# Kernel optimization log

Hardware: AMD Instinct MI355X
Metric: run time of the kernel (lower is better)

Reference implementation:

```python
import jax, jax.numpy as jnp
import numpy as np
from functools import partial

NUM_ITERS = 3
NUM_CAPS = 8      # primary capsule count
NUM_CLASSES = 10
OUT_CH = 16       # digit capsule dim
INPUT_SIZE = 32 * 6 * 6  # 1152 primary capsule units per capsule map


def squash(s, axis=-1):
    # faithful to non_linear_squashing: s * (||s||^2/(1+||s||^2)) / (||s||+1e-10)
    norm_sqr = jnp.sum(s * s, axis=axis, keepdims=True)
    scale = jnp.sqrt(norm_sqr) + 1e-10
    mag = norm_sqr / (1.0 + norm_sqr)
    return s * mag / scale


def conv2d(x, w, b, stride):
    y = jax.lax.conv_general_dilated(
        x, w, window_strides=(stride, stride), padding='VALID',
        dimension_numbers=('NCHW', 'OIHW', 'NCHW'))
    return y + b[None, :, None, None]


def setup_inputs() -> dict:
    key = jax.random.key(0)
    ks = jax.random.split(key, 6)
    B = 256
    x = jax.random.normal(ks[0], (B, 1, 28, 28), dtype=jnp.float32)
    conv_w = jax.random.normal(ks[1], (256, 1, 9, 9), dtype=jnp.float32) * 0.05
    conv_b = jax.random.normal(ks[2], (256,), dtype=jnp.float32) * 0.05
    # 8 primary capsule conv units (256->32 each) fused into one 256->256 conv
    prim_w = jax.random.normal(ks[3], (NUM_CAPS * 32, 256, 9, 9), dtype=jnp.float32) * 0.02
    prim_b = jax.random.normal(ks[4], (NUM_CAPS * 32,), dtype=jnp.float32) * 0.02
    # digit routing weights (input_size, num_classes, out_channels, num_capsules)
    digit_w = jax.random.normal(ks[5], (INPUT_SIZE, NUM_CLASSES, OUT_CH, NUM_CAPS), dtype=jnp.float32)
    return {'x': x, 'conv_w': conv_w, 'conv_b': conv_b,
            'prim_w': prim_w, 'prim_b': prim_b, 'digit_w': digit_w}


def reference(x, conv_w, conv_b, prim_w, prim_b, digit_w):
    B = x.shape[0]
    # conv stack: 1->256 k9 s1 + ReLU  (28 -> 20); pool is MaxPool2d(1,1) = identity
    h = jax.nn.relu(conv2d(x, conv_w, conv_b, stride=1))  # (B,256,20,20)
    # primary capsules: 8 convs 256->32 k9 s2, no activation (nl_activation=False)
    p = conv2d(h, prim_w, prim_b, stride=2)               # (B,256,6,6)
    u = p.reshape(B, NUM_CAPS, -1)                        # (B,8,1152)
    u = squash(u, axis=-1)
    # digit layer with dynamic routing
    # u_i: (B, IS, 8);  u_j_i[b,i,c,o] = sum_k W[i,c,o,k] * u_i[b,i,k]
    u_i = jnp.transpose(u, (0, 2, 1))                     # (B,1152,8)
    u_j_i = jnp.einsum('icok,bik->bico', digit_w, u_i)    # (B,1152,10,16)
    b_ij = jnp.zeros((INPUT_SIZE, NUM_CLASSES), dtype=x.dtype)
    out = None
    for _ in range(NUM_ITERS):
        c_ij = jax.nn.softmax(b_ij, axis=0)               # softmax over input capsules (dim=1 in torch)
        s_j = jnp.einsum('ic,bico->bco', c_ij, u_j_i)     # (B,10,16)
        # original squashes (B,1,C,16,1) along dim=2 == the CLASS axis
        out = squash(s_j, axis=1)                         # (B,10,16)
        # agreement: mean over batch of <u_j_i, v_j>
        u_v = jnp.einsum('bico,bco->ic', u_j_i, out) / B  # (1152,10)
        b_ij = b_ij + u_v
    # torch returns out.squeeze(1) with shape (B, C, 16, 1)
    return out[..., None]
```

## Files before the change

kernel.cpp:

```cpp
#include <hip/hip_runtime.h>
#include <cstdint>
#include <cstddef>


typedef __attribute__((ext_vector_type(8))) short short8;
typedef __attribute__((ext_vector_type(4))) float f32x4;

#define PHALF 2359296

__device__ __forceinline__ unsigned short f2bf_rn(float x) {
    unsigned u = __float_as_uint(x);
    unsigned r = (u + 0x7fffu + ((u >> 16) & 1u)) >> 16;
    return (unsigned short)r;
}

__global__ void k_pre(const float* __restrict__ x, const float* __restrict__ cw,
                      const float* __restrict__ cb, const float* __restrict__ w2,
                      unsigned short* __restrict__ h, unsigned short* __restrict__ wt) {
    __shared__ float sh[3376];
    int blk = blockIdx.x, t = threadIdx.x;
    if (blk < 2048) {
        float* img = sh;
        float* wsm = sh + 784;
        int b = blk >> 3, ocg = blk & 7;
        for (int idx = t; idx < 784; idx += 256) img[idx] = x[b * 784 + idx];
        for (int idx = t; idx < 2592; idx += 256) wsm[idx] = cw[ocg * 2592 + idx];
        __syncthreads();
        int oc_l = t & 31, g = t >> 5;
        int oc = ocg * 32 + oc_l;
        float bias = cb[oc];
        const float* wp = &wsm[oc_l * 81];
        for (int q = g; q < 100; q += 8) {
            int py = q / 5, qx = (q % 5) * 4;
            float a0 = bias, a1 = bias, a2 = bias, a3 = bias;
            #pragma unroll
            for (int ky = 0; ky < 9; ky++) {
                const float* ir = &img[(py + ky) * 28 + qx];
                float r[12];
                #pragma unroll
                for (int j = 0; j < 12; j++) r[j] = ir[j];
                #pragma unroll
                for (int kx = 0; kx < 9; kx++) {
                    float w = wp[ky * 9 + kx];
                    a0 += r[kx] * w; a1 += r[kx + 1] * w;
                    a2 += r[kx + 2] * w; a3 += r[kx + 3] * w;
                }
            }
            float v[4] = { fmaxf(a0, 0.f), fmaxf(a1, 0.f), fmaxf(a2, 0.f), fmaxf(a3, 0.f) };
            size_t base = ((size_t)b * 400 + py * 20 + qx) * 256 + oc;
            #pragma unroll
            for (int j = 0; j < 4; j++)
                h[base + (size_t)j * 256] = f2bf_rn(v[j]);
        }
    } else {
        int m2 = blk - 2048;
        int oc = m2 >> 3, icg = m2 & 7;
        float* lw2 = sh;
        for (int idx = t; idx < 2592; idx += 256) {
            int ic_l = idx / 81, k = idx % 81;
            lw2[idx] = w2[((size_t)oc * 256 + icg * 32 + ic_l) * 81 + k];
        }
        __syncthreads();
        for (int idx = t; idx < 324; idx += 256) {
            int k = idx >> 2, sl = idx & 3;
            unsigned short hi8[8];
            #pragma unroll
            for (int j = 0; j < 8; j++)
                hi8[j] = f2bf_rn(lw2[(sl * 8 + j) * 81 + k]);
            size_t o = ((size_t)(k * 256 + oc)) * 256 + icg * 32 + sl * 8;
            *(uint4*)&wt[o] = *(uint4*)hi8;
        }
    }
}

__global__ __launch_bounds__(256, 4) void k_conv2m(
    const unsigned short* __restrict__ h,
    const unsigned short* __restrict__ wt,
    float* __restrict__ p0, float* __restrict__ p1,
    float* __restrict__ p2, float* __restrict__ p3)
{
    __shared__ unsigned short smem[14336];
    const int t = threadIdx.x;
    const int w = t >> 6, l = t & 63;
    const int mb = blockIdx.x, nb = blockIdx.y, zz = blockIdx.z;
    const int half = zz >> 1, seg = zz & 1;

    const unsigned short* src;
    int nld, sbase;
    unsigned rowbase[8];
    if (w < 2) {
        src = h; nld = 6; sbase = w * 3072;
        #pragma unroll
        for (int ld = 0; ld < 6; ld++) {
            int row = w * 48 + ld * 8 + (l >> 3);
            int c = l & 7;
            int g = c ^ (row & 7);
            int P = mb * 96 + row;
            int b = P / 36, o = P % 36;
            int oy = o / 6, ox = o % 6;
            rowbase[ld] = (unsigned)((b * 400 + oy * 40 + ox * 2) * 256 + half * 128 + g * 8);
        }
    } else {
        src = wt; nld = 8; sbase = 6144 + (w - 2) * 4096;
        #pragma unroll
        for (int ld = 0; ld < 8; ld++) {
            int oc = (w - 2) * 64 + ld * 8 + (l >> 3);
            int c = l & 7;
            int g = c ^ (oc & 7);
            rowbase[ld] = (unsigned)((nb * 128 + oc) * 256 + half * 128 + g * 8);
        }
    }

    const int wm = w & 1, wn = w >> 1;
    const int lane16 = l & 15, q = l >> 4;

    f32x4 acc[3][4] = {};

    const int pos0 = seg ? 41 : 0;
    const int pos1 = seg ? 81 : 41;
    for (int pos = pos0; pos < pos1; ++pos) {
        const int ky = pos / 9, kx = pos - ky * 9;
        const unsigned kbase = (w < 2) ? (unsigned)((ky * 20 + kx) * 256)
                                       : (unsigned)(pos * 65536);
        for (int icc = 0; icc < 2; ++icc) {
            const unsigned kofs = kbase + icc * 64;
            __syncthreads();
            for (int ld = 0; ld < nld; ld++) {
                __builtin_amdgcn_global_load_lds(
                    (const __attribute__((address_space(1))) unsigned int*)(const void*)(src + rowbase[ld] + kofs),
                    (__attribute__((address_space(3))) unsigned int*)(void*)(smem + sbase + ld * 512),
                    16, 0, 0);
            }
            __syncthreads();
            #pragma unroll
            for (int ic2 = 0; ic2 < 2; ic2++) {
                short8 a[3], b[4];
                #pragma unroll
                for (int mt = 0; mt < 3; mt++) {
                    int pixL = wm * 48 + mt * 16 + lane16;
                    int ps = (ic2 * 4 + q) ^ (pixL & 7);
                    a[mt] = *(const short8*)(smem + pixL * 64 + ps * 8);
                }
                #pragma unroll
                for (int nt = 0; nt < 4; nt++) {
                    int ocL = wn * 64 + nt * 16 + lane16;
                    int ps = (ic2 * 4 + q) ^ (ocL & 7);
                    b[nt] = *(const short8*)(smem + 6144 + ocL * 64 + ps * 8);
                }
                #pragma unroll
                for (int mt = 0; mt < 3; mt++)
                    #pragma unroll
                    for (int nt = 0; nt < 4; nt++)
                        acc[mt][nt] = __builtin_amdgcn_mfma_f32_16x16x32_bf16(a[mt], b[nt], acc[mt][nt], 0, 0, 0);
            }
        }
    }

    #pragma unroll
    for (int mt = 0; mt < 3; mt++) {
        int pixG = mb * 96 + wm * 48 + mt * 16 + q * 4;
        int b = pixG / 36, p36 = pixG % 36;
        #pragma unroll
        for (int nt = 0; nt < 4; nt++) {
            int oc = nb * 128 + wn * 64 + nt * 16 + lane16;
            float* pout = (zz == 0) ? p0 : (zz == 1) ? p1 : (zz == 2) ? p2 : p3;
            *(f32x4*)&pout[((size_t)(b * 256 + oc)) * 36 + p36] = acc[mt][nt];
        }
    }
}

__global__ void k_sq1dw(const float* __restrict__ q0, const float* __restrict__ q1,
                        const float* __restrict__ q2, const float* __restrict__ q3,
                        const float* __restrict__ prim_b, float* __restrict__ U,
                        const float* __restrict__ dw, float* __restrict__ dwT2) {
    __shared__ float red[4];
    int blk = blockIdx.x, t = threadIdx.x;
    if (blk < 2048) {
        int b = blk >> 3, cap = blk & 7;
        size_t base = ((size_t)b * 256 + cap * 32) * 36;
        const float* pa = q0 + base;
        const float* pb = q1 + base;
        const float* pc = q2 + base;
        const float* pd = q3 + base;
        float v[5];
        float ss = 0.f;
        #pragma unroll
        for (int j = 0; j < 5; j++) {
            int idx = t + j * 256;
            if (idx < 1152) {
                int ch_l = idx / 36;
                float val = pa[idx] + pb[idx] + pc[idx] + pd[idx] + prim_b[cap * 32 + ch_l];
                v[j] = val; ss += val * val;
            } else v[j] = 0.f;
        }
        for (int off = 32; off; off >>= 1) ss += __shfl_down(ss, off);
        if ((t & 63) == 0) red[t >> 6] = ss;
        __syncthreads();
        float n2 = red[0] + red[1] + red[2] + red[3];
        float f = (n2 / (1.0f + n2)) / (sqrtf(n2) + 1e-10f);
        #pragma unroll
        for (int j = 0; j < 5; j++) {
            int idx = t + j * 256;
            if (idx < 1152) U[(size_t)b * 9216 + idx * 8 + cap] = v[j] * f;
        }
    } else {
        int co = blk - 2048;
        int c = co >> 4, o = co & 15;
        const float* base = dw + c * 128 + o * 8;
        float* out = dwT2 + (size_t)co * 9216;
        for (int idx = t; idx < 9216; idx += 256) {
            int i = idx >> 3, k = idx & 7;
            out[idx] = base[(size_t)i * 1280 + k];
        }
    }
}

__global__ void k_softmax(const float* __restrict__ bij, float* __restrict__ csm) {
    __shared__ float red[4];
    int c = blockIdx.x, t = threadIdx.x;
    float vals[5];
    float mx = -1e30f;
    #pragma unroll
    for (int j = 0; j < 5; j++) {
        int i = t + j * 256;
        vals[j] = (i < 1152) ? bij[i * 10 + c] : -1e30f;
        mx = fmaxf(mx, vals[j]);
    }
    for (int off = 32; off; off >>= 1) mx = fmaxf(mx, __shfl_down(mx, off));
    if ((t & 63) == 0) red[t >> 6] = mx;
    __syncthreads();
    mx = fmaxf(fmaxf(red[0], red[1]), fmaxf(red[2], red[3]));
    __syncthreads();
    float s = 0.f;
    #pragma unroll
    for (int j = 0; j < 5; j++) {
        int i = t + j * 256;
        vals[j] = (i < 1152) ? expf(vals[j] - mx) : 0.f;
        s += vals[j];
    }
    for (int off = 32; off; off >>= 1) s += __shfl_down(s, off);
    if ((t & 63) == 0) red[t >> 6] = s;
    __syncthreads();
    s = red[0] + red[1] + red[2] + red[3];
    float inv = 1.0f / s;
    #pragma unroll
    for (int j = 0; j < 5; j++) {
        int i = t + j * 256;
        if (i < 1152) csm[i * 10 + c] = vals[j] * inv;
    }
}

__global__ __launch_bounds__(256) void k_gemm1(const float* __restrict__ U,
                                               const float* __restrict__ dwT2,
                                               const float* __restrict__ csm,
                                               float* __restrict__ part,
                                               int uniform) {
    __shared__ float Us[32 * 36];
    __shared__ float WsT[5120];
    __shared__ float cl[360];
    int mb = blockIdx.x, kc = blockIdx.y, t = threadIdx.x;
    int tc = t & 15, tb = t >> 4;
    if (!uniform)
        for (int idx = t; idx < 360; idx += 256) cl[idx] = csm[kc * 360 + idx];
    const float uscale = 1.0f / 1152.0f;
    float acc[2][10] = {};
    for (int ks = 0; ks < 9; ks++) {
        __syncthreads();
        {
            int bb = t >> 3, k4 = t & 7;
            *(float4*)&Us[bb * 36 + k4 * 4] =
                *(const float4*)&U[(size_t)(mb * 32 + bb) * 9216 + kc * 288 + ks * 32 + k4 * 4];
        }
        #pragma unroll
        for (int pass = 0; pass < 5; pass++) {
            int s = t + pass * 256;
            int co = s >> 3, p = s & 7;
            int kq = p ^ (co & 7);
            int ikl = ks * 32 + kq * 4;
            float4 v = *(const float4*)&dwT2[(size_t)co * 9216 + kc * 288 + ikl];
            float sc = uniform ? uscale : cl[(ikl >> 3) * 10 + (co >> 4)];
            v.x *= sc; v.y *= sc; v.z *= sc; v.w *= sc;
            *(float4*)&WsT[s * 4] = v;
        }
        __syncthreads();
        float a0[32], a1[32];
        #pragma unroll
        for (int kq = 0; kq < 8; kq++) {
            float4 v0 = *(const float4*)&Us[(tb * 2) * 36 + kq * 4];
            float4 v1 = *(const float4*)&Us[(tb * 2 + 1) * 36 + kq * 4];
            a0[kq * 4 + 0] = v0.x; a0[kq * 4 + 1] = v0.y; a0[kq * 4 + 2] = v0.z; a0[kq * 4 + 3] = v0.w;
            a1[kq * 4 + 0] = v1.x; a1[kq * 4 + 1] = v1.y; a1[kq * 4 + 2] = v1.z; a1[kq * 4 + 3] = v1.w;
        }
        #pragma unroll
        for (int j = 0; j < 10; j++) {
            int co = tc + 16 * j;
            int cx = co & 7, cbase = co * 32;
            #pragma unroll
            for (int kq = 0; kq < 8; kq++) {
                float4 wv = *(const float4*)&WsT[cbase + ((kq ^ cx) << 2)];
                acc[0][j] += a0[kq * 4 + 0] * wv.x; acc[0][j] += a0[kq * 4 + 1] * wv.y;
                acc[0][j] += a0[kq * 4 + 2] * wv.z; acc[0][j] += a0[kq * 4 + 3] * wv.w;
                acc[1][j] += a1[kq * 4 + 0] * wv.x; acc[1][j] += a1[kq * 4 + 1] * wv.y;
                acc[1][j] += a1[kq * 4 + 2] * wv.z; acc[1][j] += a1[kq * 4 + 3] * wv.w;
            }
        }
    }
    #pragma unroll
    for (int r = 0; r < 2; r++)
        #pragma unroll
        for (int j = 0; j < 10; j++)
            part[(size_t)kc * 40960 + (mb * 32 + tb * 2 + r) * 160 + tc + 16 * j] = acc[r][j];
}

__global__ void k_redsq(const float* __restrict__ part, float* __restrict__ out,
                        float* __restrict__ outT, int writeT) {
    __shared__ float sl[160];
    __shared__ float n2s[16];
    int b = blockIdx.x, t = threadIdx.x;
    float s = 0.f;
    if (t < 160) {
        for (int kc = 0; kc < 32; kc++) s += part[(size_t)kc * 40960 + b * 160 + t];
        sl[t] = s;
    }
    __syncthreads();
    if (t < 16) {
        float n2 = 0.f;
        #pragma unroll
        for (int c = 0; c < 10; c++) { float v = sl[c * 16 + t]; n2 += v * v; }
        n2s[t] = n2;
    }
    __syncthreads();
    if (t < 160) {
        float n2 = n2s[t & 15];
        float f = (n2 / (1.0f + n2)) / (sqrtf(n2) + 1e-10f);
        float r = s * f;
        out[(size_t)b * 160 + t] = r;
        if (writeT) outT[(size_t)t * 256 + b] = r;
    }
}

__global__ __launch_bounds__(256) void k_g2uv(const float* __restrict__ U,
                                              const float* __restrict__ outTg,
                                              const float* __restrict__ dw,
                                              float* __restrict__ bij,
                                              int first) {
    __shared__ float UsT[1024];
    __shared__ float OsT[5120];
    __shared__ float dwl[5120];
    __shared__ float sb[320];
    int blk = blockIdx.x, t = threadIdx.x;
    int tc = t & 15, tm = t >> 4;
    for (int idx = t; idx < 5120; idx += 256)
        dwl[idx] = dw[(size_t)blk * 5120 + idx];
    float acc[2][10] = {};
    for (int bs = 0; bs < 256; bs += 32) {
        __syncthreads();
        {
            int r = t >> 3, c4 = t & 7;
            float4 v = *(const float4*)&U[(size_t)(bs + r) * 9216 + blk * 32 + c4 * 4];
            int hi = (r >> 2), lo = (r & 3);
            int m0 = c4 * 4;
            UsT[(m0 + 0) * 32 + ((hi ^ ((m0 + 0) & 7)) << 2) + lo] = v.x;
            UsT[(m0 + 1) * 32 + ((hi ^ ((m0 + 1) & 7)) << 2) + lo] = v.y;
            UsT[(m0 + 2) * 32 + ((hi ^ ((m0 + 2) & 7)) << 2) + lo] = v.z;
            UsT[(m0 + 3) * 32 + ((hi ^ ((m0 + 3) & 7)) << 2) + lo] = v.w;
        }
        #pragma unroll
        for (int pass = 0; pass < 5; pass++) {
            int s = t + pass * 256;
            int co = s >> 3, p = s & 7;
            int kq = p ^ (co & 7);
            *(float4*)&OsT[s * 4] =
                *(const float4*)&outTg[(size_t)co * 256 + bs + kq * 4];
        }
        __syncthreads();
        float a0[32], a1[32];
        int m0 = tm * 2, m1 = tm * 2 + 1;
        #pragma unroll
        for (int kq = 0; kq < 8; kq++) {
            float4 v0 = *(const float4*)&UsT[m0 * 32 + ((kq ^ (m0 & 7)) << 2)];
            float4 v1 = *(const float4*)&UsT[m1 * 32 + ((kq ^ (m1 & 7)) << 2)];
            a0[kq * 4 + 0] = v0.x; a0[kq * 4 + 1] = v0.y; a0[kq * 4 + 2] = v0.z; a0[kq * 4 + 3] = v0.w;
            a1[kq * 4 + 0] = v1.x; a1[kq * 4 + 1] = v1.y; a1[kq * 4 + 2] = v1.z; a1[kq * 4 + 3] = v1.w;
        }
        #pragma unroll
        for (int j = 0; j < 10; j++) {
            int co = tc + 16 * j;
            int cx = co & 7, cbase = co * 32;
            #pragma unroll
            for (int kq = 0; kq < 8; kq++) {
                float4 wv = *(const float4*)&OsT[cbase + ((kq ^ cx) << 2)];
                acc[0][j] += a0[kq * 4 + 0] * wv.x; acc[0][j] += a0[kq * 4 + 1] * wv.y;
                acc[0][j] += a0[kq * 4 + 2] * wv.z; acc[0][j] += a0[kq * 4 + 3] * wv.w;
                acc[1][j] += a1[kq * 4 + 0] * wv.x; acc[1][j] += a1[kq * 4 + 1] * wv.y;
                acc[1][j] += a1[kq * 4 + 2] * wv.z; acc[1][j] += a1[kq * 4 + 3] * wv.w;
            }
        }
    }
    #pragma unroll
    for (int r = 0; r < 2; r++) {
        int ik_l = tm * 2 + r;
        int i_l = ik_l >> 3, k = ik_l & 7;
        #pragma unroll
        for (int j = 0; j < 10; j++) {
            float v = acc[r][j] * dwl[i_l * 1280 + (j * 16 + tc) * 8 + k];
            v += __shfl_down(v, 8, 16);
            v += __shfl_down(v, 4, 16);
            v += __shfl_down(v, 2, 16);
            v += __shfl_down(v, 1, 16);
            if (tc == 0) sb[ik_l * 10 + j] = v;
        }
    }
    __syncthreads();
    if (t < 40) {
        int i_l = t / 10, c = t % 10;
        float s = 0.f;
        #pragma unroll
        for (int kk = 0; kk < 8; kk++) s += sb[(i_l * 8 + kk) * 10 + c];
        size_t o = (size_t)(blk * 4 + i_l) * 10 + c;
        float v = s * (1.0f / 256.0f);
        bij[o] = first ? v : (bij[o] + v);
    }
}

extern "C" void kernel_launch(void* const* d_in, const int* in_sizes, int n_in,
                              void* d_out, int out_size, void* d_ws, size_t ws_size,
                              hipStream_t stream) {
    const float* x      = (const float*)d_in[0];
    const float* conv_w = (const float*)d_in[1];
    const float* conv_b = (const float*)d_in[2];
    const float* prim_w = (const float*)d_in[3];
    const float* prim_b = (const float*)d_in[4];
    const float* dw     = (const float*)d_in[5];

    char* wsb = (char*)d_ws;
    unsigned short* h  = (unsigned short*)(wsb);
    float* dwT2 = (float*)(wsb);
    unsigned short* wt = (unsigned short*)(wsb + 52428800);
    float* pp0  = (float*)(wsb + 63045632);
    float* pp1  = (float*)(wsb + 72482816);
    float* U    = (float*)(wsb + 81920000);
    float* pp3  = (float*)(wsb + 91357184);
    float* part = (float*)(wsb + 97255424);
    float* csm  = (float*)(wsb + 102498304);
    float* bij  = (float*)(wsb + 102544384);
    float* outT = (float*)(wsb + 102590464);
    float* outw = (float*)(wsb + 102754304);
    float* pp2  = (float*)(wsb + 102918144);

    k_pre<<<4096, 256, 0, stream>>>(x, conv_w, conv_b, prim_w, h, wt);
    k_conv2m<<<dim3(96, 2, 4), 256, 0, stream>>>(h, wt, pp0, pp1, pp2, pp3);
    k_sq1dw<<<2208, 256, 0, stream>>>(pp0, pp1, pp2, pp3, prim_b, U, dw, dwT2);

    k_gemm1<<<dim3(8, 32), 256, 0, stream>>>(U, dwT2, csm, part, 1);
    k_redsq<<<256, 256, 0, stream>>>(part, outw, outT, 1);
    k_g2uv<<<288, 256, 0, stream>>>(U, outT, dw, bij, 1);
    k_softmax<<<10, 256, 0, stream>>>(bij, csm);
    k_gemm1<<<dim3(8, 32), 256, 0, stream>>>(U, dwT2, csm, part, 0);
    k_redsq<<<256, 256, 0, stream>>>(part, outw, outT, 1);
    k_g2uv<<<288, 256, 0, stream>>>(U, outT, dw, bij, 0);
    k_softmax<<<10, 256, 0, stream>>>(bij, csm);
    k_gemm1<<<dim3(8, 32), 256, 0, stream>>>(U, dwT2, csm, part, 0);
    k_redsq<<<256, 256, 0, stream>>>(part, (float*)d_out, outT, 0);
}
```

Baseline: 470.3 us.

## Fuse routing iterations into one persistent kernel with atomic grid barriers

Replaces the ten separate routing kernel launches (gemm, reduce-squash, agreement, softmax per iteration) with a single persistent kernel of 288 blocks that moves through the stages and separates them with a software grid barrier built on an atomic counter. The aim is to remove per-launch overhead and the idle tail between small dependent kernels. In exchange it relies on all 288 blocks being co-resident to avoid deadlock, adds spin-wait barrier cost, and leaves many blocks idle in the softmax stage. The counter is reset with a memset before each launch.

```diff
diff --git a/kernel.cpp b/kernel.cpp
--- a/kernel.cpp
+++ b/kernel.cpp
@@ -12,6 +12,18 @@
     unsigned u = __float_as_uint(x);
     unsigned r = (u + 0x7fffu + ((u >> 16) & 1u)) >> 16;
     return (unsigned short)r;
+}
+
+__device__ __forceinline__ void gridbar(unsigned* cnt, unsigned target) {
+    __syncthreads();
+    if (threadIdx.x == 0) {
+        __threadfence();
+        atomicAdd(cnt, 1u);
+        while (atomicAdd(cnt, 0u) < target)
+            __builtin_amdgcn_s_sleep(1);
+        __threadfence();
+    }
+    __syncthreads();
 }
 
 __global__ void k_pre(const float* __restrict__ x, const float* __restrict__ cw,
@@ -215,211 +227,217 @@
     }
 }
 
-__global__ void k_softmax(const float* __restrict__ bij, float* __restrict__ csm) {
-    __shared__ float red[4];
-    int c = blockIdx.x, t = threadIdx.x;
-    float vals[5];
-    float mx = -1e30f;
-    #pragma unroll
-    for (int j = 0; j < 5; j++) {
-        int i = t + j * 256;
-        vals[j] = (i < 1152) ? bij[i * 10 + c] : -1e30f;
-        mx = fmaxf(mx, vals[j]);
-    }
-    for (int off = 32; off; off >>= 1) mx = fmaxf(mx, __shfl_down(mx, off));
-    if ((t & 63) == 0) red[t >> 6] = mx;
-    __syncthreads();
-    mx = fmaxf(fmaxf(red[0], red[1]), fmaxf(red[2], red[3]));
-    __syncthreads();
-    float s = 0.f;
-    #pragma unroll
-    for (int j = 0; j < 5; j++) {
-        int i = t + j * 256;
-        vals[j] = (i < 1152) ? expf(vals[j] - mx) : 0.f;
-        s += vals[j];
-    }
-    for (int off = 32; off; off >>= 1) s += __shfl_down(s, off);
-    if ((t & 63) == 0) red[t >> 6] = s;
-    __syncthreads();
-    s = red[0] + red[1] + red[2] + red[3];
-    float inv = 1.0f / s;
-    #pragma unroll
-    for (int j = 0; j < 5; j++) {
-        int i = t + j * 256;
-        if (i < 1152) csm[i * 10 + c] = vals[j] * inv;
-    }
-}
-
-__global__ __launch_bounds__(256) void k_gemm1(const float* __restrict__ U,
-                                               const float* __restrict__ dwT2,
-                                               const float* __restrict__ csm,
-                                               float* __restrict__ part,
-                                               int uniform) {
-    __shared__ float Us[32 * 36];
-    __shared__ float WsT[5120];
-    __shared__ float cl[360];
-    int mb = blockIdx.x, kc = blockIdx.y, t = threadIdx.x;
-    int tc = t & 15, tb = t >> 4;
-    if (!uniform)
-        for (int idx = t; idx < 360; idx += 256) cl[idx] = csm[kc * 360 + idx];
-    const float uscale = 1.0f / 1152.0f;
-    float acc[2][10] = {};
-    for (int ks = 0; ks < 9; ks++) {
-        __syncthreads();
+__global__ __launch_bounds__(256, 2) void k_route2(
+    const float* __restrict__ U, const float* __restrict__ dwT2,
+    const float* __restrict__ dw, float* __restrict__ csm,
+    float* __restrict__ part, float* __restrict__ outT,
+    float* __restrict__ bij, float* __restrict__ dout,
+    unsigned* cnt)
+{
+    __shared__ float sm[11584];
+    const int blk = blockIdx.x, t = threadIdx.x;
+    const int tc = t & 15, tb = t >> 4;
+    unsigned target = 0;
+
+    for (int iter = 0; iter < 3; ++iter) {
+        const int uniform = (iter == 0);
+        if (blk < 256) {
+            const int mb = blk & 7, kc = blk >> 3;
+            float* Us  = sm;
+            float* WsT = sm + 1152;
+            float* cl  = sm + 6272;
+            if (!uniform)
+                for (int idx = t; idx < 360; idx += 256) cl[idx] = csm[kc * 360 + idx];
+            const float uscale = 1.0f / 1152.0f;
+            float acc[2][10] = {};
+            for (int ks = 0; ks < 9; ks++) {
+                __syncthreads();
+                {
+                    int bb = t >> 3, k4 = t & 7;
+                    *(float4*)&Us[bb * 36 + k4 * 4] =
+                        *(const float4*)&U[(size_t)(mb * 32 + bb) * 9216 + kc * 288 + ks * 32 + k4 * 4];
+                }
+                #pragma unroll
+                for (int pass = 0; pass < 5; pass++) {
+                    int s = t + pass * 256;
+                    int co = s >> 3, p = s & 7;
+                    int kq = p ^ (co & 7);
+                    int ikl = ks * 32 + kq * 4;
+                    float4 v = *(const float4*)&dwT2[(size_t)co * 9216 + kc * 288 + ikl];
+                    float sc = uniform ? uscale : cl[(ikl >> 3) * 10 + (co >> 4)];
+                    v.x *= sc; v.y *= sc; v.z *= sc; v.w *= sc;
+                    *(float4*)&WsT[s * 4] = v;
+                }
+                __syncthreads();
+                float a0[32], a1[32];
+                #pragma unroll
+                for (int kq = 0; kq < 8; kq++) {
+                    float4 v0 = *(const float4*)&Us[(tb * 2) * 36 + kq * 4];
+                    float4 v1 = *(const float4*)&Us[(tb * 2 + 1) * 36 + kq * 4];
+                    a0[kq * 4 + 0] = v0.x; a0[kq * 4 + 1] = v0.y; a0[kq * 4 + 2] = v0.z; a0[kq * 4 + 3] = v0.w;
+                    a1[kq * 4 + 0] = v1.x; a1[kq * 4 + 1] = v1.y; a1[kq * 4 + 2] = v1.z; a1[kq * 4 + 3] = v1.w;
+                }
+                #pragma unroll
+                for (int j = 0; j < 10; j++) {
+                    int co = tc + 16 * j;
+                    int cx = co & 7, cbase = co * 32;
+                    #pragma unroll
+                    for (int kq = 0; kq < 8; kq++) {
+                        float4 wv = *(const float4*)&WsT[cbase + ((kq ^ cx) << 2)];
+                        acc[0][j] += a0[kq * 4 + 0] * wv.x; acc[0][j] += a0[kq * 4 + 1] * wv.y;
+                        acc[0][j] += a0[kq * 4 + 2] * wv.z; acc[0][j] += a0[kq * 4 + 3] * wv.w;
+                        acc[1][j] += a1[kq * 4 + 0] * wv.x; acc[1][j] += a1[kq * 4 + 1] * wv.y;
+                        acc[1][j] += a1[kq * 4 + 2] * wv.z; acc[1][j] += a1[kq * 4 + 3] * wv.w;
+                    }
+                }
+            }
+            #pragma unroll
+            for (int r = 0; r < 2; r++)
+                #pragma unroll
+                for (int j = 0; j < 10; j++)
+                    part[(size_t)kc * 40960 + (mb * 32 + tb * 2 + r) * 160 + tc + 16 * j] = acc[r][j];
+        }
+        target += 288; gridbar(cnt, target);
+        if (blk < 256) {
+            float* sl  = sm;
+            float* n2s = sm + 160;
+            int b = blk;
+            float s = 0.f;
+            if (t < 160) {
+                for (int kc = 0; kc < 32; kc++) s += part[(size_t)kc * 40960 + b * 160 + t];
+                sl[t] = s;
+            }
+            __syncthreads();
+            if (t < 16) {
+                float n2 = 0.f;
+                #pragma unroll
+                for (int c = 0; c < 10; c++) { float v = sl[c * 16 + t]; n2 += v * v; }
+                n2s[t] = n2;
+            }
+            __syncthreads();
+            if (t < 160) {
+                float n2 = n2s[t & 15];
+                float f = (n2 / (1.0f + n2)) / (sqrtf(n2) + 1e-10f);
+                float r = s * f;
+                if (iter == 2) dout[(size_t)b * 160 + t] = r;
+                else           outT[(size_t)t * 256 + b] = r;
+            }
+        }
+        if (iter == 2) return;
+        target += 288; gridbar(cnt, target);
         {
-            int bb = t >> 3, k4 = t & 7;
-            *(float4*)&Us[bb * 36 + k4 * 4] =
-                *(const float4*)&U[(size_t)(mb * 32 + bb) * 9216 + kc * 288 + ks * 32 + k4 * 4];
-        }
-        #pragma unroll
-        for (int pass = 0; pass < 5; pass++) {
-            int s = t + pass * 256;
-            int co = s >> 3, p = s & 7;
-            int kq = p ^ (co & 7);
-            int ikl = ks * 32 + kq * 4;
-            float4 v = *(const float4*)&dwT2[(size_t)co * 9216 + kc * 288 + ikl];
-            float sc = uniform ? uscale : cl[(ikl >> 3) * 10 + (co >> 4)];
-            v.x *= sc; v.y *= sc; v.z *= sc; v.w *= sc;
-            *(float4*)&WsT[s * 4] = v;
-        }
-        __syncthreads();
-        float a0[32], a1[32];
-        #pragma unroll
-        for (int kq = 0; kq < 8; kq++) {
-            float4 v0 = *(const float4*)&Us[(tb * 2) * 36 + kq * 4];
-            float4 v1 = *(const float4*)&Us[(tb * 2 + 1) * 36 + kq * 4];
-            a0[kq * 4 + 0] = v0.x; a0[kq * 4 + 1] = v0.y; a0[kq * 4 + 2] = v0.z; a0[kq * 4 + 3] = v0.w;
-            a1[kq * 4 + 0] = v1.x; a1[kq * 4 + 1] = v1.y; a1[kq * 4 + 2] = v1.z; a1[kq * 4 + 3] = v1.w;
-        }
-        #pragma unroll
-        for (int j = 0; j < 10; j++) {
-            int co = tc + 16 * j;
-            int cx = co & 7, cbase = co * 32;
-            #pragma unroll
-            for (int kq = 0; kq < 8; kq++) {
-                float4 wv = *(const float4*)&WsT[cbase + ((kq ^ cx) << 2)];
-                acc[0][j] += a0[kq * 4 + 0] * wv.x; acc[0][j] += a0[kq * 4 + 1] * wv.y;
-                acc[0][j] += a0[kq * 4 + 2] * wv.z; acc[0][j] += a0[kq * 4 + 3] * wv.w;
-                acc[1][j] += a1[kq * 4 + 0] * wv.x; acc[1][j] += a1[kq * 4 + 1] * wv.y;
-                acc[1][j] += a1[kq * 4 + 2] * wv.z; acc[1][j] += a1[kq * 4 + 3] * wv.w;
-            }
-        }
-    }
-    #pragma unroll
-    for (int r = 0; r < 2; r++)
-        #pragma unroll
-        for (int j = 0; j < 10; j++)
-            part[(size_t)kc * 40960 + (mb * 32 + tb * 2 + r) * 160 + tc + 16 * j] = acc[r][j];
-}
-
-__global__ void k_redsq(const float* __restrict__ part, float* __restrict__ out,
-                        float* __restrict__ outT, int writeT) {
-    __shared__ float sl[160];
-    __shared__ float n2s[16];
-    int b = blockIdx.x, t = threadIdx.x;
-    float s = 0.f;
-    if (t < 160) {
-        for (int kc = 0; kc < 32; kc++) s += part[(size_t)kc * 40960 + b * 160 + t];
-        sl[t] = s;
-    }
-    __syncthreads();
-    if (t < 16) {
-        float n2 = 0.f;
-        #pragma unroll
-        for (int c = 0; c < 10; c++) { float v = sl[c * 16 + t]; n2 += v * v; }
-        n2s[t] = n2;
-    }
-    __syncthreads();
-    if (t < 160) {
-        float n2 = n2s[t & 15];
-        float f = (n2 / (1.0f + n2)) / (sqrtf(n2) + 1e-10f);
-        float r = s * f;
-        out[(size_t)b * 160 + t] = r;
-        if (writeT) outT[(size_t)t * 256 + b] = r;
-    }
-}
-
-__global__ __launch_bounds__(256) void k_g2uv(const float* __restrict__ U,
-                                              const float* __restrict__ outTg,
-                                              const float* __restrict__ dw,
-                                              float* __restrict__ bij,
-                                              int first) {
-    __shared__ float UsT[1024];
-    __shared__ float OsT[5120];
-    __shared__ float dwl[5120];
-    __shared__ float sb[320];
-    int blk = blockIdx.x, t = threadIdx.x;
-    int tc = t & 15, tm = t >> 4;
-    for (int idx = t; idx < 5120; idx += 256)
-        dwl[idx] = dw[(size_t)blk * 5120 + idx];
-    float acc[2][10] = {};
-    for (int bs = 0; bs < 256; bs += 32) {
-        __syncthreads();
-        {
-            int r = t >> 3, c4 = t & 7;
-            float4 v = *(const float4*)&U[(size_t)(bs + r) * 9216 + blk * 32 + c4 * 4];
-            int hi = (r >> 2), lo = (r & 3);
-            int m0 = c4 * 4;
-            UsT[(m0 + 0) * 32 + ((hi ^ ((m0 + 0) & 7)) << 2) + lo] = v.x;
-            UsT[(m0 + 1) * 32 + ((hi ^ ((m0 + 1) & 7)) << 2) + lo] = v.y;
-            UsT[(m0 + 2) * 32 + ((hi ^ ((m0 + 2) & 7)) << 2) + lo] = v.z;
-            UsT[(m0 + 3) * 32 + ((hi ^ ((m0 + 3) & 7)) << 2) + lo] = v.w;
-        }
-        #pragma unroll
-        for (int pass = 0; pass < 5; pass++) {
-            int s = t + pass * 256;
-            int co = s >> 3, p = s & 7;
-            int kq = p ^ (co & 7);
-            *(float4*)&OsT[s * 4] =
-                *(const float4*)&outTg[(size_t)co * 256 + bs + kq * 4];
-        }
-        __syncthreads();
-        float a0[32], a1[32];
-        int m0 = tm * 2, m1 = tm * 2 + 1;
-        #pragma unroll
-        for (int kq = 0; kq < 8; kq++) {
-            float4 v0 = *(const float4*)&UsT[m0 * 32 + ((kq ^ (m0 & 7)) << 2)];
-            float4 v1 = *(const float4*)&UsT[m1 * 32 + ((kq ^ (m1 & 7)) << 2)];
-            a0[kq * 4 + 0] = v0.x; a0[kq * 4 + 1] = v0.y; a0[kq * 4 + 2] = v0.z; a0[kq * 4 + 3] = v0.w;
-            a1[kq * 4 + 0] = v1.x; a1[kq * 4 + 1] = v1.y; a1[kq * 4 + 2] = v1.z; a1[kq * 4 + 3] = v1.w;
-        }
-        #pragma unroll
-        for (int j = 0; j < 10; j++) {
-            int co = tc + 16 * j;
-            int cx = co & 7, cbase = co * 32;
-            #pragma unroll
-            for (int kq = 0; kq < 8; kq++) {
-                float4 wv = *(const float4*)&OsT[cbase + ((kq ^ cx) << 2)];
-                acc[0][j] += a0[kq * 4 + 0] * wv.x; acc[0][j] += a0[kq * 4 + 1] * wv.y;
-                acc[0][j] += a0[kq * 4 + 2] * wv.z; acc[0][j] += a0[kq * 4 + 3] * wv.w;
-                acc[1][j] += a1[kq * 4 + 0] * wv.x; acc[1][j] += a1[kq * 4 + 1] * wv.y;
-                acc[1][j] += a1[kq * 4 + 2] * wv.z; acc[1][j] += a1[kq * 4 + 3] * wv.w;
-            }
-        }
-    }
-    #pragma unroll
-    for (int r = 0; r < 2; r++) {
-        int ik_l = tm * 2 + r;
-        int i_l = ik_l >> 3, k = ik_l & 7;
-        #pragma unroll
-        for (int j = 0; j < 10; j++) {
-            float v = acc[r][j] * dwl[i_l * 1280 + (j * 16 + tc) * 8 + k];
-            v += __shfl_down(v, 8, 16);
-            v += __shfl_down(v, 4, 16);
-            v += __shfl_down(v, 2, 16);
-            v += __shfl_down(v, 1, 16);
-            if (tc == 0) sb[ik_l * 10 + j] = v;
-        }
-    }
-    __syncthreads();
-    if (t < 40) {
-        int i_l = t / 10, c = t % 10;
-        float s = 0.f;
-        #pragma unroll
-        for (int kk = 0; kk < 8; kk++) s += sb[(i_l * 8 + kk) * 10 + c];
-        size_t o = (size_t)(blk * 4 + i_l) * 10 + c;
-        float v = s * (1.0f / 256.0f);
-        bij[o] = first ? v : (bij[o] + v);
+            float* UsT = sm;
+            float* OsT = sm + 1024;
+            float* dwl = sm + 6144;
+            float* sb  = sm + 11264;
+            for (int idx = t; idx < 5120; idx += 256)
+                dwl[idx] = dw[(size_t)blk * 5120 + idx];
+            float acc[2][10] = {};
+            for (int bs = 0; bs < 256; bs += 32) {
+                __syncthreads();
+                {
+                    int r = t >> 3, c4 = t & 7;
+                    float4 v = *(const float4*)&U[(size_t)(bs + r) * 9216 + blk * 32 + c4 * 4];
+                    int hi = (r >> 2), lo = (r & 3);
+                    int m0 = c4 * 4;
+                    UsT[(m0 + 0) * 32 + ((hi ^ ((m0 + 0) & 7)) << 2) + lo] = v.x;
+                    UsT[(m0 + 1) * 32 + ((hi ^ ((m0 + 1) & 7)) << 2) + lo] = v.y;
+                    UsT[(m0 + 2) * 32 + ((hi ^ ((m0 + 2) & 7)) << 2) + lo] = v.z;
+                    UsT[(m0 + 3) * 32 + ((hi ^ ((m0 + 3) & 7)) << 2) + lo] = v.w;
+                }
+                #pragma unroll
+                for (int pass = 0; pass < 5; pass++) {
+                    int s = t + pass * 256;
+                    int co = s >> 3, p = s & 7;
+                    int kq = p ^ (co & 7);
+                    *(float4*)&OsT[s * 4] =
+                        *(const float4*)&outT[(size_t)co * 256 + bs + kq * 4];
+                }
+                __syncthreads();
+                float a0[32], a1[32];
+                int m0 = tb * 2, m1 = tb * 2 + 1;
+                #pragma unroll
+                for (int kq = 0; kq < 8; kq++) {
+                    float4 v0 = *(const float4*)&UsT[m0 * 32 + ((kq ^ (m0 & 7)) << 2)];
+                    float4 v1 = *(const float4*)&UsT[m1 * 32 + ((kq ^ (m1 & 7)) << 2)];
+                    a0[kq * 4 + 0] = v0.x; a0[kq * 4 + 1] = v0.y; a0[kq * 4 + 2] = v0.z; a0[kq * 4 + 3] = v0.w;
+                    a1[kq * 4 + 0] = v1.x; a1[kq * 4 + 1] = v1.y; a1[kq * 4 + 2] = v1.z; a1[kq * 4 + 3] = v1.w;
+                }
+                #pragma unroll
+                for (int j = 0; j < 10; j++) {
+                    int co = tc + 16 * j;
+                    int cx = co & 7, cbase = co * 32;
+                    #pragma unroll
+                    for (int kq = 0; kq < 8; kq++) {
+                        float4 wv = *(const float4*)&OsT[cbase + ((kq ^ cx) << 2)];
+                        acc[0][j] += a0[kq * 4 + 0] * wv.x; acc[0][j] += a0[kq * 4 + 1] * wv.y;
+                        acc[0][j] += a0[kq * 4 + 2] * wv.z; acc[0][j] += a0[kq * 4 + 3] * wv.w;
+                        acc[1][j] += a1[kq * 4 + 0] * wv.x; acc[1][j] += a1[kq * 4 + 1] * wv.y;
+                        acc[1][j] += a1[kq * 4 + 2] * wv.z; acc[1][j] += a1[kq * 4 + 3] * wv.w;
+                    }
+                }
+            }
+            #pragma unroll
+            for (int r = 0; r < 2; r++) {
+                int ik_l = tb * 2 + r;
+                int i_l = ik_l >> 3, k = ik_l & 7;
+                #pragma unroll
+                for (int j = 0; j < 10; j++) {
+                    float v = acc[r][j] * dwl[i_l * 1280 + (j * 16 + tc) * 8 + k];
+                    v += __shfl_down(v, 8, 16);
+                    v += __shfl_down(v, 4, 16);
+                    v += __shfl_down(v, 2, 16);
+                    v += __shfl_down(v, 1, 16);
+                    if (tc == 0) sb[ik_l * 10 + j] = v;
+                }
+            }
+            __syncthreads();
+            if (t < 40) {
+                int i_l = t / 10, c = t % 10;
+                float s = 0.f;
+                #pragma unroll
+                for (int kk = 0; kk < 8; kk++) s += sb[(i_l * 8 + kk) * 10 + c];
+                size_t o = (size_t)(blk * 4 + i_l) * 10 + c;
+                float v = s * (1.0f / 256.0f);
+                bij[o] = uniform ? v : (bij[o] + v);
+            }
+        }
+        target += 288; gridbar(cnt, target);
+        if (blk < 10) {
+            float* red = sm;
+            int c = blk;
+            float vals[5];
+            float mx = -1e30f;
+            #pragma unroll
+            for (int j = 0; j < 5; j++) {
+                int i = t + j * 256;
+                vals[j] = (i < 1152) ? bij[i * 10 + c] : -1e30f;
+                mx = fmaxf(mx, vals[j]);
+            }
+            for (int off = 32; off; off >>= 1) mx = fmaxf(mx, __shfl_down(mx, off));
+            if ((t & 63) == 0) red[t >> 6] = mx;
+            __syncthreads();
+            mx = fmaxf(fmaxf(red[0], red[1]), fmaxf(red[2], red[3]));
+            __syncthreads();
+            float s = 0.f;
+            #pragma unroll
+            for (int j = 0; j < 5; j++) {
+                int i = t + j * 256;
+                vals[j] = (i < 1152) ? expf(vals[j] - mx) : 0.f;
+                s += vals[j];
+            }
+            for (int off = 32; off; off >>= 1) s += __shfl_down(s, off);
+            if ((t & 63) == 0) red[t >> 6] = s;
+            __syncthreads();
+            s = red[0] + red[1] + red[2] + red[3];
+            float inv = 1.0f / s;
+            #pragma unroll
+            for (int j = 0; j < 5; j++) {
+                int i = t + j * 256;
+                if (i < 1152) csm[i * 10 + c] = vals[j] * inv;
+            }
+        }
+        target += 288; gridbar(cnt, target);
     }
 }
 
@@ -445,21 +463,13 @@
     float* csm  = (float*)(wsb + 102498304);
     float* bij  = (float*)(wsb + 102544384);
     float* outT = (float*)(wsb + 102590464);
-    float* outw = (float*)(wsb + 102754304);
+    unsigned* cnt = (unsigned*)(wsb + 102754304);
     float* pp2  = (float*)(wsb + 102918144);
+    float* dout = (float*)d_out;
 
     k_pre<<<4096, 256, 0, stream>>>(x, conv_w, conv_b, prim_w, h, wt);
     k_conv2m<<<dim3(96, 2, 4), 256, 0, stream>>>(h, wt, pp0, pp1, pp2, pp3);
     k_sq1dw<<<2208, 256, 0, stream>>>(pp0, pp1, pp2, pp3, prim_b, U, dw, dwT2);
-
-    k_gemm1<<<dim3(8, 32), 256, 0, stream>>>(U, dwT2, csm, part, 1);
-    k_redsq<<<256, 256, 0, stream>>>(part, outw, outT, 1);
-    k_g2uv<<<288, 256, 0, stream>>>(U, outT, dw, bij, 1);
-    k_softmax<<<10, 256, 0, stream>>>(bij, csm);
-    k_gemm1<<<dim3(8, 32), 256, 0, stream>>>(U, dwT2, csm, part, 0);
-    k_redsq<<<256, 256, 0, stream>>>(part, outw, outT, 1);
-    k_g2uv<<<288, 256, 0, stream>>>(U, outT, dw, bij, 0);
-    k_softmax<<<10, 256, 0, stream>>>(bij, csm);
-    k_gemm1<<<dim3(8, 32), 256, 0, stream>>>(U, dwT2, csm, part, 0);
-    k_redsq<<<256, 256, 0, stream>>>(part, (float*)d_out, outT, 0);
-}
+    hipMemsetAsync(cnt, 0, sizeof(unsigned), stream);
+    k_route2<<<288, 256, 0, stream>>>(U, dwT2, dw, csm, part, outT, bij, dout, cnt);
+}
```

New measurement: 731.5 us. 55.5% more time.

## Restructure conv1 so each thread owns two pixels and writes 16-byte bf16 vectors

Applied to the files above, without the earlier changes.

The first conv in the prep kernel now assigns each of 200 threads a pair of output pixels. Each thread keeps a 9x10 input window in registers and loops over the block's 32 output channels, reading weights directly from global memory (uniform across the wave) instead of staging them in shared memory. Outputs are packed eight channels at a time into 16-byte stores, replacing the scattered 2-byte stores. The trade-offs are heavier register use, 56 idle threads per block, and serial per-channel work on each thread.

```diff
diff --git a/kernel.cpp b/kernel.cpp
--- a/kernel.cpp
+++ b/kernel.cpp
@@ -14,43 +14,48 @@
     return (unsigned short)r;
 }
 
-__global__ void k_pre(const float* __restrict__ x, const float* __restrict__ cw,
-                      const float* __restrict__ cb, const float* __restrict__ w2,
-                      unsigned short* __restrict__ h, unsigned short* __restrict__ wt) {
-    __shared__ float sh[3376];
+__global__ __launch_bounds__(256) void k_pre(
+    const float* __restrict__ x, const float* __restrict__ cw,
+    const float* __restrict__ cb, const float* __restrict__ w2,
+    unsigned short* __restrict__ h, unsigned short* __restrict__ wt) {
+    __shared__ float sh[2592];
     int blk = blockIdx.x, t = threadIdx.x;
     if (blk < 2048) {
         float* img = sh;
-        float* wsm = sh + 784;
         int b = blk >> 3, ocg = blk & 7;
         for (int idx = t; idx < 784; idx += 256) img[idx] = x[b * 784 + idx];
-        for (int idx = t; idx < 2592; idx += 256) wsm[idx] = cw[ocg * 2592 + idx];
-        __syncthreads();
-        int oc_l = t & 31, g = t >> 5;
-        int oc = ocg * 32 + oc_l;
-        float bias = cb[oc];
-        const float* wp = &wsm[oc_l * 81];
-        for (int q = g; q < 100; q += 8) {
-            int py = q / 5, qx = (q % 5) * 4;
-            float a0 = bias, a1 = bias, a2 = bias, a3 = bias;
+        __syncthreads();
+        if (t < 200) {
+            int py = t / 10, qx = (t % 10) * 2;
+            float win[9][10];
             #pragma unroll
-            for (int ky = 0; ky < 9; ky++) {
-                const float* ir = &img[(py + ky) * 28 + qx];
-                float r[12];
+            for (int ky = 0; ky < 9; ky++)
                 #pragma unroll
-                for (int j = 0; j < 12; j++) r[j] = ir[j];
+                for (int c = 0; c < 10; c++)
+                    win[ky][c] = img[(py + ky) * 28 + qx + c];
+            size_t base0 = ((size_t)b * 400 + py * 20 + qx) * 256 + ocg * 32;
+            size_t base1 = base0 + 256;
+            for (int oc8 = 0; oc8 < 4; ++oc8) {
+                unsigned short hb0[8], hb1[8];
                 #pragma unroll
-                for (int kx = 0; kx < 9; kx++) {
-                    float w = wp[ky * 9 + kx];
-                    a0 += r[kx] * w; a1 += r[kx + 1] * w;
-                    a2 += r[kx + 2] * w; a3 += r[kx + 3] * w;
+                for (int j = 0; j < 8; j++) {
+                    int oc = ocg * 32 + oc8 * 8 + j;
+                    const float* wp = cw + oc * 81;
+                    float a0 = cb[oc], a1 = a0;
+                    #pragma unroll
+                    for (int ky = 0; ky < 9; ky++)
+                        #pragma unroll
+                        for (int kx = 0; kx < 9; kx++) {
+                            float w = wp[ky * 9 + kx];
+                            a0 += win[ky][kx] * w;
+                            a1 += win[ky][kx + 1] * w;
+                        }
+                    hb0[j] = f2bf_rn(fmaxf(a0, 0.f));
+                    hb1[j] = f2bf_rn(fmaxf(a1, 0.f));
                 }
+                *(uint4*)&h[base0 + oc8 * 8] = *(uint4*)hb0;
+                *(uint4*)&h[base1 + oc8 * 8] = *(uint4*)hb1;
             }
-            float v[4] = { fmaxf(a0, 0.f), fmaxf(a1, 0.f), fmaxf(a2, 0.f), fmaxf(a3, 0.f) };
-            size_t base = ((size_t)b * 400 + py * 20 + qx) * 256 + oc;
-            #pragma unroll
-            for (int j = 0; j < 4; j++)
-                h[base + (size_t)j * 256] = f2bf_rn(v[j]);
         }
     } else {
         int m2 = blk - 2048;
```

New measurement: 549.1 us. 1.17x slower.
